# Performance work log

Measured on AMD Instinct MI355X. Metric: run time of the kernel, lower is better.

## Reference

```python
import jax, jax.numpy as jnp
import numpy as np

DIM = 512
DIM_HEAD = 64
HEADS = 8
DIM_INNER = DIM_HEAD * HEADS
EPS = float(jnp.finfo(jnp.float32).eps)  # torch nn.RMSNorm default eps


def setup_inputs() -> dict:
    key = jax.random.key(0)
    k1, k2, k3, k4 = jax.random.split(key, 4)
    tokens = jax.random.normal(k1, (2, 4096, DIM), dtype=jnp.float32)
    norm_weight = jnp.ones((DIM,), dtype=jnp.float32)
    s = 1.0 / np.sqrt(DIM)
    w_qkv = jax.random.normal(k2, (DIM, 3 * DIM_INNER), dtype=jnp.float32) * s
    w_out = jax.random.normal(k3, (DIM_INNER, DIM), dtype=jnp.float32) * (1.0 / np.sqrt(DIM_INNER))
    return {"tokens": tokens, "norm_weight": norm_weight, "w_qkv": w_qkv, "w_out": w_out}


def reference(tokens, norm_weight, w_qkv, w_out):
    b, n, d = tokens.shape
    scale = DIM_HEAD ** -0.5
    # RMSNorm
    ms = jnp.mean(jnp.square(tokens), axis=-1, keepdims=True)
    x = tokens * jax.lax.rsqrt(ms + EPS) * norm_weight
    # QKV projection, split heads: b n (qkv h d) -> qkv b h n d
    qkv = x @ w_qkv                                   # [b, n, 3*h*dh]
    qkv = qkv.reshape(b, n, 3, HEADS, DIM_HEAD)
    q, k, v = jnp.moveaxis(qkv, 2, 0)                 # each [b, n, h, dh]
    q = jnp.swapaxes(q, 1, 2)                         # [b, h, n, dh]
    k = jnp.swapaxes(k, 1, 2)
    v = jnp.swapaxes(v, 1, 2)
    # naive attention (note: original applies no scale in forward, self.scale unused)
    sim = jnp.einsum('bhid,bhjd->bhij', q, k)
    attn = jax.nn.softmax(sim, axis=-1)
    out = jnp.einsum('bhij,bhjd->bhid', attn, v)
    out = jnp.swapaxes(out, 1, 2).reshape(b, n, DIM_INNER)
    return out @ w_out
```

## Files before the change

kernel.cpp:

```cpp
#include <hip/hip_runtime.h>
#include <stdint.h>
#include <stddef.h>

typedef _Float16 half_t;
typedef __attribute__((ext_vector_type(2))) __fp16 fp16v2;
typedef __attribute__((ext_vector_type(4))) _Float16 f16x4;
typedef __attribute__((ext_vector_type(8))) _Float16 f16x8;
typedef __attribute__((ext_vector_type(4))) float f32x4;

#define EPSF 1.1920928955078125e-07f
#define LOG2E 1.4426950408889634f

#define AS1 __attribute__((address_space(1)))
#define AS3 __attribute__((address_space(3)))

#define WS_XN   0u
#define WS_WQT  4194304u
#define WS_WOT  4980736u
#define WS_Q    5242880u
#define WS_K    9437184u
#define WS_VT   13631488u
#define WS_AO   17825792u
#define WS_NEED_BYTES 44040192u

__device__ __forceinline__ void gload16(const void* g, void* l) {
  __builtin_amdgcn_global_load_lds((const AS1 void*)g, (AS3 void*)l, 16, 0, 0);
}

__device__ __forceinline__ float fast_exp2(float x) {
#if __has_builtin(__builtin_amdgcn_exp2f)
  return __builtin_amdgcn_exp2f(x);
#else
  return exp2f(x);
#endif
}

__global__ __launch_bounds__(256) void k_rmsnorm(const float* __restrict__ t,
                                                 const float* __restrict__ w,
                                                 half_t* __restrict__ xn) {
  int row = blockIdx.x * 4 + (threadIdx.x >> 6);
  int ln = threadIdx.x & 63;
  const float* src = t + (size_t)row * 512 + ln * 8;
  float4 a = *(const float4*)src;
  float4 b = *(const float4*)(src + 4);
  float ss = a.x * a.x + a.y * a.y + a.z * a.z + a.w * a.w
           + b.x * b.x + b.y * b.y + b.z * b.z + b.w * b.w;
#pragma unroll
  for (int m = 32; m >= 1; m >>= 1) ss += __shfl_xor(ss, m);
  float r = rsqrtf(ss * (1.0f / 512.0f) + EPSF);
  const float* wp = w + ln * 8;
  float4 w0 = *(const float4*)wp;
  float4 w1 = *(const float4*)(wp + 4);
  f16x8 o;
  o[0] = (_Float16)(a.x * r * w0.x);
  o[1] = (_Float16)(a.y * r * w0.y);
  o[2] = (_Float16)(a.z * r * w0.z);
  o[3] = (_Float16)(a.w * r * w0.w);
  o[4] = (_Float16)(b.x * r * w1.x);
  o[5] = (_Float16)(b.y * r * w1.y);
  o[6] = (_Float16)(b.z * r * w1.z);
  o[7] = (_Float16)(b.w * r * w1.w);
  *(f16x8*)(xn + (size_t)row * 512 + ln * 8) = o;
}

__global__ void k_transpose_cast(const float* __restrict__ src, half_t* __restrict__ dst,
                                 int K, int N) {
  int idx = blockIdx.x * 256 + threadIdx.x;
  if (idx >= K * N) return;
  int n = idx / K, k = idx - n * K;
  dst[idx] = (_Float16)src[(size_t)k * N + n];
}

__device__ __forceinline__ void gemm_core(const half_t* __restrict__ A,
                                          const half_t* __restrict__ Bt,
                                          int m0, int n0, int Ksz,
                                          half_t* Al, half_t* Bl,
                                          f32x4 acc[4][4]) {
  int wv = threadIdx.x >> 6, ln = threadIdx.x & 63;
  int wm = (wv >> 1) << 6, wn = (wv & 1) << 6;
  for (int kt = 0; kt < Ksz; kt += 64) {
#pragma unroll
    for (int i = 0; i < 4; ++i) {
      int seg = wv * 4 + i;
      int r = seg * 8 + (ln >> 3);
      int cb = ((ln & 7) * 16) ^ ((r & 7) << 4);
      gload16((const char*)(A + (size_t)(m0 + r) * Ksz + kt) + cb, (char*)Al + seg * 1024);
      gload16((const char*)(Bt + (size_t)(n0 + r) * Ksz + kt) + cb, (char*)Bl + seg * 1024);
    }
    __syncthreads();
#pragma unroll
    for (int kc = 0; kc < 2; ++kc) {
      f16x8 af[4], bf[4];
#pragma unroll
      for (int mt = 0; mt < 4; ++mt) {
        int rr = wm + mt * 16 + (ln & 15);
        af[mt] = *(const f16x8*)((const char*)Al + rr * 128 +
                                 ((kc * 64 + (ln >> 4) * 16) ^ ((rr & 7) << 4)));
      }
#pragma unroll
      for (int nt = 0; nt < 4; ++nt) {
        int rr = wn + nt * 16 + (ln & 15);
        bf[nt] = *(const f16x8*)((const char*)Bl + rr * 128 +
                                 ((kc * 64 + (ln >> 4) * 16) ^ ((rr & 7) << 4)));
      }
#pragma unroll
      for (int mt = 0; mt < 4; ++mt)
#pragma unroll
        for (int nt = 0; nt < 4; ++nt)
          acc[mt][nt] = __builtin_amdgcn_mfma_f32_16x16x32_f16(af[mt], bf[nt], acc[mt][nt], 0, 0, 0);
    }
    __syncthreads();
  }
}

__global__ __launch_bounds__(256, 2) void k_gemm_qkv(const half_t* __restrict__ A,
                                                     const half_t* __restrict__ Bt,
                                                     half_t* __restrict__ q,
                                                     half_t* __restrict__ kk,
                                                     half_t* __restrict__ vt) {
  __shared__ __align__(16) half_t Al[128 * 64];
  __shared__ __align__(16) half_t Bl[128 * 64];
  f32x4 acc[4][4];
  f32x4 z = {0.f, 0.f, 0.f, 0.f};
#pragma unroll
  for (int i = 0; i < 4; ++i)
#pragma unroll
    for (int j = 0; j < 4; ++j) acc[i][j] = z;
  int m0 = blockIdx.x * 128, n0 = blockIdx.y * 128;
  gemm_core(A, Bt, m0, n0, 512, Al, Bl, acc);
  int wv = threadIdx.x >> 6, ln = threadIdx.x & 63;
  int wm = (wv >> 1) << 6, wn = (wv & 1) << 6;
#pragma unroll
  for (int mt = 0; mt < 4; ++mt) {
#pragma unroll
    for (int nt = 0; nt < 4; ++nt) {
      int gn = n0 + wn + nt * 16 + (ln & 15);
      int qkv_i = gn >> 9;
      int h = (gn >> 6) & 7;
      int d = gn & 63;
#pragma unroll
      for (int j = 0; j < 4; ++j) {
        int gm = m0 + wm + mt * 16 + (ln >> 4) * 4 + j;
        int head = ((gm >> 12) << 3) | h;
        int n = gm & 4095;
        float av = acc[mt][nt][j];
        if (qkv_i == 0)      q [((size_t)head * 4096 + n) * 64 + d] = (_Float16)(av * LOG2E);
        else if (qkv_i == 1) kk[((size_t)head * 4096 + n) * 64 + d] = (_Float16)av;
        else {
          int pcol = (n & ~31) | (((n >> 2) & 3) << 3) | (((n >> 4) & 1) << 2) | (n & 3);
          vt[((size_t)head * 64 + d) * 4096 + pcol] = (_Float16)av;
        }
      }
    }
  }
}

__global__ __launch_bounds__(256, 2) void k_gemm_out(const half_t* __restrict__ A,
                                                     const half_t* __restrict__ Bt,
                                                     float* __restrict__ out) {
  __shared__ __align__(16) half_t Al[128 * 64];
  __shared__ __align__(16) half_t Bl[128 * 64];
  f32x4 acc[4][4];
  f32x4 z = {0.f, 0.f, 0.f, 0.f};
#pragma unroll
  for (int i = 0; i < 4; ++i)
#pragma unroll
    for (int j = 0; j < 4; ++j) acc[i][j] = z;
  int m0 = blockIdx.x * 128, n0 = blockIdx.y * 128;
  gemm_core(A, Bt, m0, n0, 512, Al, Bl, acc);
  int wv = threadIdx.x >> 6, ln = threadIdx.x & 63;
  int wm = (wv >> 1) << 6, wn = (wv & 1) << 6;
#pragma unroll
  for (int mt = 0; mt < 4; ++mt)
#pragma unroll
    for (int nt = 0; nt < 4; ++nt) {
      int gn = n0 + wn + nt * 16 + (ln & 15);
#pragma unroll
      for (int j = 0; j < 4; ++j) {
        int gm = m0 + wm + mt * 16 + (ln >> 4) * 4 + j;
        out[(size_t)gm * 512 + gn] = acc[mt][nt][j];
      }
    }
}

__global__ __launch_bounds__(256, 2) void k_attn(const half_t* __restrict__ q,
                                                 const half_t* __restrict__ kg,
                                                 const half_t* __restrict__ vt,
                                                 half_t* __restrict__ ao) {
  __shared__ __align__(16) char lds[32768];
  const int wv = threadIdx.x >> 6, ln = threadIdx.x & 63;
  const int bid = blockIdx.x;
  const int lin = (bid & 7) * 64 + (bid >> 3);
  const int head = lin >> 5;
  const int qt = lin & 31;
  const int q0 = qt * 128 + wv * 32;
  const char* qh = (const char*)(q  + (size_t)head * 4096 * 64);
  const char* kh = (const char*)(kg + (size_t)head * 4096 * 64);
  const char* vh = (const char*)(vt + (size_t)head * 64 * 4096);

  f16x8 qf[2][2];
#pragma unroll
  for (int mt = 0; mt < 2; ++mt)
#pragma unroll
    for (int kc = 0; kc < 2; ++kc) {
      int r = q0 + mt * 16 + (ln & 15);
      qf[mt][kc] = *(const f16x8*)(qh + (size_t)r * 128 + kc * 64 + (ln >> 4) * 16);
    }

  const char* ks[2]; const char* vs[2]; int lo[2];
#pragma unroll
  for (int i = 0; i < 2; ++i) {
    int seg = wv * 2 + i;
    int r = seg * 8 + (ln >> 3);
    int cb = ((ln & 7) * 16) ^ ((r & 7) << 4);
    ks[i] = kh + (size_t)r * 128 + cb;
    vs[i] = vh + (size_t)r * 8192 + cb;
    lo[i] = seg * 1024;
  }

  float mrun[2] = {-1e30f, -1e30f};
  f32x4 oacc[2][4];
  f32x4 lacc[2];
  const f32x4 z = {0.f, 0.f, 0.f, 0.f};
#pragma unroll
  for (int mt = 0; mt < 2; ++mt) {
    lacc[mt] = z;
#pragma unroll
    for (int dt = 0; dt < 4; ++dt) oacc[mt][dt] = z;
  }
  f16x8 ones;
#pragma unroll
  for (int e = 0; e < 8; ++e) ones[e] = (_Float16)1.0f;

  {
    char* base = lds;
    gload16(ks[0], base + lo[0]); gload16(ks[1], base + lo[1]);
    gload16(vs[0], base + 8192 + lo[0]); gload16(vs[1], base + 8192 + lo[1]);
    ks[0] += 8192; ks[1] += 8192; vs[0] += 128; vs[1] += 128;
  }
  __syncthreads();

  int cur = 0;
#pragma unroll 1
  for (int t = 0; t < 64; ++t) {
    if (t < 63) {
      char* base = lds + (cur ^ 1) * 16384;
      gload16(ks[0], base + lo[0]); gload16(ks[1], base + lo[1]);
      gload16(vs[0], base + 8192 + lo[0]); gload16(vs[1], base + 8192 + lo[1]);
      ks[0] += 8192; ks[1] += 8192; vs[0] += 128; vs[1] += 128;
    }
    const char* Kb = lds + cur * 16384;
    const char* Vb = Kb + 8192;

    f32x4 s[2][4];
#pragma unroll
    for (int mt = 0; mt < 2; ++mt)
#pragma unroll
      for (int kt = 0; kt < 4; ++kt) s[mt][kt] = z;
    __builtin_amdgcn_s_setprio(1);
#pragma unroll
    for (int kc = 0; kc < 2; ++kc) {
      f16x8 kf[4];
#pragma unroll
      for (int kt = 0; kt < 4; ++kt) {
        int rr = kt * 16 + (ln & 15);
        kf[kt] = *(const f16x8*)(Kb + rr * 128 + ((kc * 64 + (ln >> 4) * 16) ^ ((rr & 7) << 4)));
      }
#pragma unroll
      for (int mt = 0; mt < 2; ++mt)
#pragma unroll
        for (int kt = 0; kt < 4; ++kt)
          s[mt][kt] = __builtin_amdgcn_mfma_f32_16x16x32_f16(kf[kt], qf[mt][kc], s[mt][kt], 0, 0, 0);
    }
    __builtin_amdgcn_s_setprio(0);

    f16x8 vf[2][4];
#pragma unroll
    for (int dt = 0; dt < 4; ++dt) {
      int rr = dt * 16 + (ln & 15);
      int sw = (rr & 7) << 4;
      vf[0][dt] = *(const f16x8*)(Vb + rr * 128 + (((ln >> 4) * 16) ^ sw));
      vf[1][dt] = *(const f16x8*)(Vb + rr * 128 + ((64 + (ln >> 4) * 16) ^ sw));
    }

    f16x8 pf[2][2];
#pragma unroll
    for (int mt = 0; mt < 2; ++mt) {
      float a0 = fmaxf(fmaxf(s[mt][0][0], s[mt][0][1]), fmaxf(s[mt][0][2], s[mt][0][3]));
      float a1 = fmaxf(fmaxf(s[mt][1][0], s[mt][1][1]), fmaxf(s[mt][1][2], s[mt][1][3]));
      float a2 = fmaxf(fmaxf(s[mt][2][0], s[mt][2][1]), fmaxf(s[mt][2][2], s[mt][2][3]));
      float a3 = fmaxf(fmaxf(s[mt][3][0], s[mt][3][1]), fmaxf(s[mt][3][2], s[mt][3][3]));
      float tm = fmaxf(fmaxf(a0, a1), fmaxf(a2, a3));
      tm = fmaxf(tm, __shfl_xor(tm, 16));
      tm = fmaxf(tm, __shfl_xor(tm, 32));
      if (__any(tm > mrun[mt] + 11.0f)) {
        float mnew = fmaxf(mrun[mt], tm);
        float sc = fast_exp2(mrun[mt] - mnew);
        mrun[mt] = mnew;
        lacc[mt][0] *= sc;
#pragma unroll
        for (int dt = 0; dt < 4; ++dt) {
          oacc[mt][dt][0] *= sc; oacc[mt][dt][1] *= sc;
          oacc[mt][dt][2] *= sc; oacc[mt][dt][3] *= sc;
        }
      }
      float p[4][4];
#pragma unroll
      for (int kt = 0; kt < 4; ++kt)
#pragma unroll
        for (int r = 0; r < 4; ++r) p[kt][r] = fast_exp2(s[mt][kt][r] - mrun[mt]);
#pragma unroll
      for (int kc = 0; kc < 2; ++kc) {
        union { f16x8 v; fp16v2 h[4]; } u;
        u.h[0] = __builtin_amdgcn_cvt_pkrtz(p[2 * kc][0], p[2 * kc][1]);
        u.h[1] = __builtin_amdgcn_cvt_pkrtz(p[2 * kc][2], p[2 * kc][3]);
        u.h[2] = __builtin_amdgcn_cvt_pkrtz(p[2 * kc + 1][0], p[2 * kc + 1][1]);
        u.h[3] = __builtin_amdgcn_cvt_pkrtz(p[2 * kc + 1][2], p[2 * kc + 1][3]);
        pf[mt][kc] = u.v;
      }
    }

    __builtin_amdgcn_s_setprio(1);
#pragma unroll
    for (int dt = 0; dt < 4; ++dt)
#pragma unroll
      for (int mt = 0; mt < 2; ++mt)
        oacc[mt][dt] = __builtin_amdgcn_mfma_f32_16x16x32_f16(vf[0][dt], pf[mt][0], oacc[mt][dt], 0, 0, 0);
    lacc[0] = __builtin_amdgcn_mfma_f32_16x16x32_f16(ones, pf[0][0], lacc[0], 0, 0, 0);
    lacc[1] = __builtin_amdgcn_mfma_f32_16x16x32_f16(ones, pf[1][0], lacc[1], 0, 0, 0);
#pragma unroll
    for (int dt = 0; dt < 4; ++dt)
#pragma unroll
      for (int mt = 0; mt < 2; ++mt)
        oacc[mt][dt] = __builtin_amdgcn_mfma_f32_16x16x32_f16(vf[1][dt], pf[mt][1], oacc[mt][dt], 0, 0, 0);
    lacc[0] = __builtin_amdgcn_mfma_f32_16x16x32_f16(ones, pf[0][1], lacc[0], 0, 0, 0);
    lacc[1] = __builtin_amdgcn_mfma_f32_16x16x32_f16(ones, pf[1][1], lacc[1], 0, 0, 0);
    __builtin_amdgcn_s_setprio(0);

    __syncthreads();
    cur ^= 1;
  }

  const int b = head >> 3, h = head & 7;
#pragma unroll
  for (int mt = 0; mt < 2; ++mt) {
    float inv = 1.0f / lacc[mt][0];
    int n = q0 + mt * 16 + (ln & 15);
    half_t* dst = ao + ((size_t)(b * 4096 + n)) * 512 + h * 64 + (ln >> 4) * 4;
#pragma unroll
    for (int dt = 0; dt < 4; ++dt) {
      f16x4 o4;
      o4[0] = (_Float16)(oacc[mt][dt][0] * inv);
      o4[1] = (_Float16)(oacc[mt][dt][1] * inv);
      o4[2] = (_Float16)(oacc[mt][dt][2] * inv);
      o4[3] = (_Float16)(oacc[mt][dt][3] * inv);
      *(f16x4*)(dst + dt * 16) = o4;
    }
  }
}

extern "C" void kernel_launch(void* const* d_in, const int* in_sizes, int n_in,
                              void* d_out, int out_size, void* d_ws, size_t ws_size,
                              hipStream_t stream) {
  if (ws_size < WS_NEED_BYTES) return;
  const float* tokens = (const float*)d_in[0];
  const float* nw     = (const float*)d_in[1];
  const float* wqkv   = (const float*)d_in[2];
  const float* wout   = (const float*)d_in[3];
  float* out = (float*)d_out;
  half_t* ws = (half_t*)d_ws;
  half_t* xn  = ws + WS_XN;
  half_t* wqt = ws + WS_WQT;
  half_t* wot = ws + WS_WOT;
  half_t* qb  = ws + WS_Q;
  half_t* kb  = ws + WS_K;
  half_t* vtb = ws + WS_VT;
  half_t* aob = ws + WS_AO;

  k_rmsnorm<<<2048, 256, 0, stream>>>(tokens, nw, xn);
  k_transpose_cast<<<(1536 * 512 + 255) / 256, 256, 0, stream>>>(wqkv, wqt, 512, 1536);
  k_transpose_cast<<<(512 * 512 + 255) / 256, 256, 0, stream>>>(wout, wot, 512, 512);
  k_gemm_qkv<<<dim3(64, 12), 256, 0, stream>>>(xn, wqt, qb, kb, vtb);
  k_attn<<<512, 256, 0, stream>>>(qb, kb, vtb, aob);
  k_gemm_out<<<dim3(64, 4), 256, 0, stream>>>(aob, wot, out);
}
```

Before: 142.9 us.

## Split attention query rows across 8 waves and fuse weight transposes via LDS

```diff
diff --git a/kernel.cpp b/kernel.cpp
--- a/kernel.cpp
+++ b/kernel.cpp
@@ -63,12 +63,28 @@
   *(f16x8*)(xn + (size_t)row * 512 + ln * 8) = o;
 }
 
-__global__ void k_transpose_cast(const float* __restrict__ src, half_t* __restrict__ dst,
-                                 int K, int N) {
-  int idx = blockIdx.x * 256 + threadIdx.x;
-  if (idx >= K * N) return;
-  int n = idx / K, k = idx - n * K;
-  dst[idx] = (_Float16)src[(size_t)k * N + n];
+__global__ __launch_bounds__(256) void k_wtrans(const float* __restrict__ wqkv,
+                                                const float* __restrict__ wout,
+                                                half_t* __restrict__ wqt,
+                                                half_t* __restrict__ wot) {
+  __shared__ half_t tile[64][65];
+  int b = blockIdx.x;
+  const float* src; half_t* dst; int N, tk, tn;
+  if (b < 192) { src = wqkv; dst = wqt; N = 1536; tk = b / 24; tn = b - tk * 24; }
+  else { b -= 192; src = wout; dst = wot; N = 512; tk = b >> 3; tn = b & 7; }
+  int c = threadIdx.x & 63;
+  int r0 = threadIdx.x >> 6;
+#pragma unroll
+  for (int i = 0; i < 16; ++i) {
+    int r = i * 4 + r0;
+    tile[r][c] = (_Float16)src[(size_t)(tk * 64 + r) * N + tn * 64 + c];
+  }
+  __syncthreads();
+#pragma unroll
+  for (int i = 0; i < 16; ++i) {
+    int n = i * 4 + r0;
+    dst[(size_t)(tn * 64 + n) * 512 + tk * 64 + c] = tile[c][n];
+  }
 }
 
 __device__ __forceinline__ void gemm_core(const half_t* __restrict__ A,
@@ -183,7 +199,7 @@
     }
 }
 
-__global__ __launch_bounds__(256, 2) void k_attn(const half_t* __restrict__ q,
+__global__ __launch_bounds__(512, 4) void k_attn(const half_t* __restrict__ q,
                                                  const half_t* __restrict__ kg,
                                                  const half_t* __restrict__ vt,
                                                  half_t* __restrict__ ao) {
@@ -193,51 +209,38 @@
   const int lin = (bid & 7) * 64 + (bid >> 3);
   const int head = lin >> 5;
   const int qt = lin & 31;
-  const int q0 = qt * 128 + wv * 32;
+  const int q0 = qt * 128 + wv * 16;
   const char* qh = (const char*)(q  + (size_t)head * 4096 * 64);
   const char* kh = (const char*)(kg + (size_t)head * 4096 * 64);
   const char* vh = (const char*)(vt + (size_t)head * 64 * 4096);
 
-  f16x8 qf[2][2];
-#pragma unroll
-  for (int mt = 0; mt < 2; ++mt)
-#pragma unroll
-    for (int kc = 0; kc < 2; ++kc) {
-      int r = q0 + mt * 16 + (ln & 15);
-      qf[mt][kc] = *(const f16x8*)(qh + (size_t)r * 128 + kc * 64 + (ln >> 4) * 16);
-    }
-
-  const char* ks[2]; const char* vs[2]; int lo[2];
-#pragma unroll
-  for (int i = 0; i < 2; ++i) {
-    int seg = wv * 2 + i;
-    int r = seg * 8 + (ln >> 3);
-    int cb = ((ln & 7) * 16) ^ ((r & 7) << 4);
-    ks[i] = kh + (size_t)r * 128 + cb;
-    vs[i] = vh + (size_t)r * 8192 + cb;
-    lo[i] = seg * 1024;
-  }
-
-  float mrun[2] = {-1e30f, -1e30f};
-  f32x4 oacc[2][4];
-  f32x4 lacc[2];
+  f16x8 qf[2];
+#pragma unroll
+  for (int kc = 0; kc < 2; ++kc) {
+    int r = q0 + (ln & 15);
+    qf[kc] = *(const f16x8*)(qh + (size_t)r * 128 + kc * 64 + (ln >> 4) * 16);
+  }
+
+  const int sr = wv * 8 + (ln >> 3);
+  const int cb = ((ln & 7) * 16) ^ ((sr & 7) << 4);
+  const char* ks = kh + (size_t)sr * 128 + cb;
+  const char* vs = vh + (size_t)sr * 8192 + cb;
+  const int lo = wv * 1024;
+
+  float mrun = -1e30f;
+  f32x4 oacc[4];
+  f32x4 lacc;
   const f32x4 z = {0.f, 0.f, 0.f, 0.f};
-#pragma unroll
-  for (int mt = 0; mt < 2; ++mt) {
-    lacc[mt] = z;
-#pragma unroll
-    for (int dt = 0; dt < 4; ++dt) oacc[mt][dt] = z;
-  }
+  lacc = z;
+#pragma unroll
+  for (int dt = 0; dt < 4; ++dt) oacc[dt] = z;
   f16x8 ones;
 #pragma unroll
   for (int e = 0; e < 8; ++e) ones[e] = (_Float16)1.0f;
 
-  {
-    char* base = lds;
-    gload16(ks[0], base + lo[0]); gload16(ks[1], base + lo[1]);
-    gload16(vs[0], base + 8192 + lo[0]); gload16(vs[1], base + 8192 + lo[1]);
-    ks[0] += 8192; ks[1] += 8192; vs[0] += 128; vs[1] += 128;
-  }
+  gload16(ks, lds + lo);
+  gload16(vs, lds + 8192 + lo);
+  ks += 8192; vs += 128;
   __syncthreads();
 
   int cur = 0;
@@ -245,18 +248,16 @@
   for (int t = 0; t < 64; ++t) {
     if (t < 63) {
       char* base = lds + (cur ^ 1) * 16384;
-      gload16(ks[0], base + lo[0]); gload16(ks[1], base + lo[1]);
-      gload16(vs[0], base + 8192 + lo[0]); gload16(vs[1], base + 8192 + lo[1]);
-      ks[0] += 8192; ks[1] += 8192; vs[0] += 128; vs[1] += 128;
+      gload16(ks, base + lo);
+      gload16(vs, base + 8192 + lo);
+      ks += 8192; vs += 128;
     }
     const char* Kb = lds + cur * 16384;
     const char* Vb = Kb + 8192;
 
-    f32x4 s[2][4];
-#pragma unroll
-    for (int mt = 0; mt < 2; ++mt)
-#pragma unroll
-      for (int kt = 0; kt < 4; ++kt) s[mt][kt] = z;
+    f32x4 s[4];
+#pragma unroll
+    for (int kt = 0; kt < 4; ++kt) s[kt] = z;
     __builtin_amdgcn_s_setprio(1);
 #pragma unroll
     for (int kc = 0; kc < 2; ++kc) {
@@ -267,10 +268,8 @@
         kf[kt] = *(const f16x8*)(Kb + rr * 128 + ((kc * 64 + (ln >> 4) * 16) ^ ((rr & 7) << 4)));
       }
 #pragma unroll
-      for (int mt = 0; mt < 2; ++mt)
-#pragma unroll
-        for (int kt = 0; kt < 4; ++kt)
-          s[mt][kt] = __builtin_amdgcn_mfma_f32_16x16x32_f16(kf[kt], qf[mt][kc], s[mt][kt], 0, 0, 0);
+      for (int kt = 0; kt < 4; ++kt)
+        s[kt] = __builtin_amdgcn_mfma_f32_16x16x32_f16(kf[kt], qf[kc], s[kt], 0, 0, 0);
     }
     __builtin_amdgcn_s_setprio(0);
 
@@ -283,32 +282,31 @@
       vf[1][dt] = *(const f16x8*)(Vb + rr * 128 + ((64 + (ln >> 4) * 16) ^ sw));
     }
 
-    f16x8 pf[2][2];
-#pragma unroll
-    for (int mt = 0; mt < 2; ++mt) {
-      float a0 = fmaxf(fmaxf(s[mt][0][0], s[mt][0][1]), fmaxf(s[mt][0][2], s[mt][0][3]));
-      float a1 = fmaxf(fmaxf(s[mt][1][0], s[mt][1][1]), fmaxf(s[mt][1][2], s[mt][1][3]));
-      float a2 = fmaxf(fmaxf(s[mt][2][0], s[mt][2][1]), fmaxf(s[mt][2][2], s[mt][2][3]));
-      float a3 = fmaxf(fmaxf(s[mt][3][0], s[mt][3][1]), fmaxf(s[mt][3][2], s[mt][3][3]));
+    f16x8 pf[2];
+    {
+      float a0 = fmaxf(fmaxf(s[0][0], s[0][1]), fmaxf(s[0][2], s[0][3]));
+      float a1 = fmaxf(fmaxf(s[1][0], s[1][1]), fmaxf(s[1][2], s[1][3]));
+      float a2 = fmaxf(fmaxf(s[2][0], s[2][1]), fmaxf(s[2][2], s[2][3]));
+      float a3 = fmaxf(fmaxf(s[3][0], s[3][1]), fmaxf(s[3][2], s[3][3]));
       float tm = fmaxf(fmaxf(a0, a1), fmaxf(a2, a3));
       tm = fmaxf(tm, __shfl_xor(tm, 16));
       tm = fmaxf(tm, __shfl_xor(tm, 32));
-      if (__any(tm > mrun[mt] + 11.0f)) {
-        float mnew = fmaxf(mrun[mt], tm);
-        float sc = fast_exp2(mrun[mt] - mnew);
-        mrun[mt] = mnew;
-        lacc[mt][0] *= sc;
+      if (__any(tm > mrun + 11.0f)) {
+        float mnew = fmaxf(mrun, tm);
+        float sc = fast_exp2(mrun - mnew);
+        mrun = mnew;
+        lacc[0] *= sc;
 #pragma unroll
         for (int dt = 0; dt < 4; ++dt) {
-          oacc[mt][dt][0] *= sc; oacc[mt][dt][1] *= sc;
-          oacc[mt][dt][2] *= sc; oacc[mt][dt][3] *= sc;
+          oacc[dt][0] *= sc; oacc[dt][1] *= sc;
+          oacc[dt][2] *= sc; oacc[dt][3] *= sc;
         }
       }
       float p[4][4];
 #pragma unroll
       for (int kt = 0; kt < 4; ++kt)
 #pragma unroll
-        for (int r = 0; r < 4; ++r) p[kt][r] = fast_exp2(s[mt][kt][r] - mrun[mt]);
+        for (int r = 0; r < 4; ++r) p[kt][r] = fast_exp2(s[kt][r] - mrun);
 #pragma unroll
       for (int kc = 0; kc < 2; ++kc) {
         union { f16x8 v; fp16v2 h[4]; } u;
@@ -316,25 +314,19 @@
         u.h[1] = __builtin_amdgcn_cvt_pkrtz(p[2 * kc][2], p[2 * kc][3]);
         u.h[2] = __builtin_amdgcn_cvt_pkrtz(p[2 * kc + 1][0], p[2 * kc + 1][1]);
         u.h[3] = __builtin_amdgcn_cvt_pkrtz(p[2 * kc + 1][2], p[2 * kc + 1][3]);
-        pf[mt][kc] = u.v;
+        pf[kc] = u.v;
       }
     }
 
     __builtin_amdgcn_s_setprio(1);
 #pragma unroll
     for (int dt = 0; dt < 4; ++dt)
-#pragma unroll
-      for (int mt = 0; mt < 2; ++mt)
-        oacc[mt][dt] = __builtin_amdgcn_mfma_f32_16x16x32_f16(vf[0][dt], pf[mt][0], oacc[mt][dt], 0, 0, 0);
-    lacc[0] = __builtin_amdgcn_mfma_f32_16x16x32_f16(ones, pf[0][0], lacc[0], 0, 0, 0);
-    lacc[1] = __builtin_amdgcn_mfma_f32_16x16x32_f16(ones, pf[1][0], lacc[1], 0, 0, 0);
+      oacc[dt] = __builtin_amdgcn_mfma_f32_16x16x32_f16(vf[0][dt], pf[0], oacc[dt], 0, 0, 0);
+    lacc = __builtin_amdgcn_mfma_f32_16x16x32_f16(ones, pf[0], lacc, 0, 0, 0);
 #pragma unroll
     for (int dt = 0; dt < 4; ++dt)
-#pragma unroll
-      for (int mt = 0; mt < 2; ++mt)
-        oacc[mt][dt] = __builtin_amdgcn_mfma_f32_16x16x32_f16(vf[1][dt], pf[mt][1], oacc[mt][dt], 0, 0, 0);
-    lacc[0] = __builtin_amdgcn_mfma_f32_16x16x32_f16(ones, pf[0][1], lacc[0], 0, 0, 0);
-    lacc[1] = __builtin_amdgcn_mfma_f32_16x16x32_f16(ones, pf[1][1], lacc[1], 0, 0, 0);
+      oacc[dt] = __builtin_amdgcn_mfma_f32_16x16x32_f16(vf[1][dt], pf[1], oacc[dt], 0, 0, 0);
+    lacc = __builtin_amdgcn_mfma_f32_16x16x32_f16(ones, pf[1], lacc, 0, 0, 0);
     __builtin_amdgcn_s_setprio(0);
 
     __syncthreads();
@@ -342,18 +334,17 @@
   }
 
   const int b = head >> 3, h = head & 7;
-#pragma unroll
-  for (int mt = 0; mt < 2; ++mt) {
-    float inv = 1.0f / lacc[mt][0];
-    int n = q0 + mt * 16 + (ln & 15);
+  {
+    float inv = 1.0f / lacc[0];
+    int n = q0 + (ln & 15);
     half_t* dst = ao + ((size_t)(b * 4096 + n)) * 512 + h * 64 + (ln >> 4) * 4;
 #pragma unroll
     for (int dt = 0; dt < 4; ++dt) {
       f16x4 o4;
-      o4[0] = (_Float16)(oacc[mt][dt][0] * inv);
-      o4[1] = (_Float16)(oacc[mt][dt][1] * inv);
-      o4[2] = (_Float16)(oacc[mt][dt][2] * inv);
-      o4[3] = (_Float16)(oacc[mt][dt][3] * inv);
+      o4[0] = (_Float16)(oacc[dt][0] * inv);
+      o4[1] = (_Float16)(oacc[dt][1] * inv);
+      o4[2] = (_Float16)(oacc[dt][2] * inv);
+      o4[3] = (_Float16)(oacc[dt][3] * inv);
       *(f16x4*)(dst + dt * 16) = o4;
     }
   }
@@ -378,9 +369,8 @@
   half_t* aob = ws + WS_AO;
 
   k_rmsnorm<<<2048, 256, 0, stream>>>(tokens, nw, xn);
-  k_transpose_cast<<<(1536 * 512 + 255) / 256, 256, 0, stream>>>(wqkv, wqt, 512, 1536);
-  k_transpose_cast<<<(512 * 512 + 255) / 256, 256, 0, stream>>>(wout, wot, 512, 512);
+  k_wtrans<<<256, 256, 0, stream>>>(wqkv, wout, wqt, wot);
   k_gemm_qkv<<<dim3(64, 12), 256, 0, stream>>>(xn, wqt, qb, kb, vtb);
-  k_attn<<<512, 256, 0, stream>>>(qb, kb, vtb, aob);
+  k_attn<<<512, 512, 0, stream>>>(qb, kb, vtb, aob);
   k_gemm_out<<<dim3(64, 4), 256, 0, stream>>>(aob, wot, out);
 }
```

Result: faster. 135.4 us (-5.2%).

## Tile weight transpose in LDS and fold running max into QK accumulator init

Applied to the files above, without the earlier changes.

```diff
diff --git a/kernel.cpp b/kernel.cpp
--- a/kernel.cpp
+++ b/kernel.cpp
@@ -63,12 +63,28 @@
   *(f16x8*)(xn + (size_t)row * 512 + ln * 8) = o;
 }
 
-__global__ void k_transpose_cast(const float* __restrict__ src, half_t* __restrict__ dst,
-                                 int K, int N) {
-  int idx = blockIdx.x * 256 + threadIdx.x;
-  if (idx >= K * N) return;
-  int n = idx / K, k = idx - n * K;
-  dst[idx] = (_Float16)src[(size_t)k * N + n];
+__global__ __launch_bounds__(256) void k_wtrans(const float* __restrict__ wqkv,
+                                                const float* __restrict__ wout,
+                                                half_t* __restrict__ wqt,
+                                                half_t* __restrict__ wot) {
+  __shared__ half_t tile[64][65];
+  int b = blockIdx.x;
+  const float* src; half_t* dst; int N, tk, tn;
+  if (b < 192) { src = wqkv; dst = wqt; N = 1536; tk = b / 24; tn = b - tk * 24; }
+  else { b -= 192; src = wout; dst = wot; N = 512; tk = b >> 3; tn = b & 7; }
+  int c = threadIdx.x & 63;
+  int r0 = threadIdx.x >> 6;
+#pragma unroll
+  for (int i = 0; i < 16; ++i) {
+    int r = i * 4 + r0;
+    tile[r][c] = (_Float16)src[(size_t)(tk * 64 + r) * N + tn * 64 + c];
+  }
+  __syncthreads();
+#pragma unroll
+  for (int i = 0; i < 16; ++i) {
+    int n = i * 4 + r0;
+    dst[(size_t)(tn * 64 + n) * 512 + tk * 64 + c] = tile[c][n];
+  }
 }
 
 __device__ __forceinline__ void gemm_core(const half_t* __restrict__ A,
@@ -218,7 +234,7 @@
     lo[i] = seg * 1024;
   }
 
-  float mrun[2] = {-1e30f, -1e30f};
+  float mrun[2] = {0.0f, 0.0f};
   f32x4 oacc[2][4];
   f32x4 lacc[2];
   const f32x4 z = {0.f, 0.f, 0.f, 0.f};
@@ -254,9 +270,11 @@
 
     f32x4 s[2][4];
 #pragma unroll
-    for (int mt = 0; mt < 2; ++mt)
-#pragma unroll
-      for (int kt = 0; kt < 4; ++kt) s[mt][kt] = z;
+    for (int mt = 0; mt < 2; ++mt) {
+      float nm = -mrun[mt];
+      f32x4 mi = {nm, nm, nm, nm};
+      s[mt][0] = mi; s[mt][1] = mi; s[mt][2] = mi; s[mt][3] = mi;
+    }
     __builtin_amdgcn_s_setprio(1);
 #pragma unroll
     for (int kc = 0; kc < 2; ++kc) {
@@ -286,29 +304,36 @@
     f16x8 pf[2][2];
 #pragma unroll
     for (int mt = 0; mt < 2; ++mt) {
-      float a0 = fmaxf(fmaxf(s[mt][0][0], s[mt][0][1]), fmaxf(s[mt][0][2], s[mt][0][3]));
-      float a1 = fmaxf(fmaxf(s[mt][1][0], s[mt][1][1]), fmaxf(s[mt][1][2], s[mt][1][3]));
-      float a2 = fmaxf(fmaxf(s[mt][2][0], s[mt][2][1]), fmaxf(s[mt][2][2], s[mt][2][3]));
-      float a3 = fmaxf(fmaxf(s[mt][3][0], s[mt][3][1]), fmaxf(s[mt][3][2], s[mt][3][3]));
-      float tm = fmaxf(fmaxf(a0, a1), fmaxf(a2, a3));
+      float m0_ = fmaxf(fmaxf(s[mt][0][0], s[mt][0][1]), s[mt][0][2]);
+      float m1_ = fmaxf(fmaxf(s[mt][0][3], s[mt][1][0]), s[mt][1][1]);
+      float m2_ = fmaxf(fmaxf(s[mt][1][2], s[mt][1][3]), s[mt][2][0]);
+      float m3_ = fmaxf(fmaxf(s[mt][2][1], s[mt][2][2]), s[mt][2][3]);
+      float m4_ = fmaxf(fmaxf(s[mt][3][0], s[mt][3][1]), s[mt][3][2]);
+      float m5_ = fmaxf(fmaxf(m0_, m1_), m2_);
+      float tm = fmaxf(fmaxf(fmaxf(m3_, m4_), s[mt][3][3]), m5_);
       tm = fmaxf(tm, __shfl_xor(tm, 16));
       tm = fmaxf(tm, __shfl_xor(tm, 32));
-      if (__any(tm > mrun[mt] + 11.0f)) {
-        float mnew = fmaxf(mrun[mt], tm);
-        float sc = fast_exp2(mrun[mt] - mnew);
-        mrun[mt] = mnew;
+      float p[4][4];
+      if (__any(tm > 11.0f)) {
+        float dlt = fmaxf(tm, 0.0f);
+        float sc = fast_exp2(-dlt);
+        mrun[mt] += dlt;
         lacc[mt][0] *= sc;
 #pragma unroll
         for (int dt = 0; dt < 4; ++dt) {
           oacc[mt][dt][0] *= sc; oacc[mt][dt][1] *= sc;
           oacc[mt][dt][2] *= sc; oacc[mt][dt][3] *= sc;
         }
-      }
-      float p[4][4];
-#pragma unroll
-      for (int kt = 0; kt < 4; ++kt)
-#pragma unroll
-        for (int r = 0; r < 4; ++r) p[kt][r] = fast_exp2(s[mt][kt][r] - mrun[mt]);
+#pragma unroll
+        for (int kt = 0; kt < 4; ++kt)
+#pragma unroll
+          for (int r = 0; r < 4; ++r) p[kt][r] = fast_exp2(s[mt][kt][r] - dlt);
+      } else {
+#pragma unroll
+        for (int kt = 0; kt < 4; ++kt)
+#pragma unroll
+          for (int r = 0; r < 4; ++r) p[kt][r] = fast_exp2(s[mt][kt][r]);
+      }
 #pragma unroll
       for (int kc = 0; kc < 2; ++kc) {
         union { f16x8 v; fp16v2 h[4]; } u;
@@ -378,8 +403,7 @@
   half_t* aob = ws + WS_AO;
 
   k_rmsnorm<<<2048, 256, 0, stream>>>(tokens, nw, xn);
-  k_transpose_cast<<<(1536 * 512 + 255) / 256, 256, 0, stream>>>(wqkv, wqt, 512, 1536);
-  k_transpose_cast<<<(512 * 512 + 255) / 256, 256, 0, stream>>>(wout, wot, 512, 512);
+  k_wtrans<<<256, 256, 0, stream>>>(wqkv, wout, wqt, wot);
   k_gemm_qkv<<<dim3(64, 12), 256, 0, stream>>>(xn, wqt, qb, kb, vtb);
   k_attn<<<512, 256, 0, stream>>>(qb, kb, vtb, aob);
   k_gemm_out<<<dim3(64, 4), 256, 0, stream>>>(aob, wot, out);
```

Result: faster. 135.1 us (-5.5%).
